# Optimization experiments

Measured on AMD Instinct MI355X. Metric: run time of the kernel, lower is better.

Reference implementation:

```python
import jax, jax.numpy as jnp
import numpy as np

B, N, C, H, R = 64, 197, 768, 12, 98   # batch, tokens, dim, heads, eliminated tokens
SPARSITY, ALPHA = 0.2, 0.1
EPS = 1e-5  # torch nn.LayerNorm default


def layernorm(x, g, b):
    m = jnp.mean(x, axis=-1, keepdims=True)
    v = jnp.var(x, axis=-1, keepdims=True)
    return (x - m) / jnp.sqrt(v + EPS) * g + b


def setup_inputs() -> dict:
    key = jax.random.key(0)
    ks = jax.random.split(key, 8)
    s = lambda k, sh: (jax.random.normal(k, sh, jnp.float32) * 0.02)
    return dict(
        x=jax.random.normal(ks[0], (B, N, C), jnp.float32),
        norm1_g=jnp.ones((C,), jnp.float32), norm1_b=jnp.zeros((C,), jnp.float32),
        qkv_w=s(ks[1], (C, 3 * C)),                      # qkv_bias=False
        proj_w=s(ks[2], (C, C)), proj_b=jnp.zeros((C,), jnp.float32),
        norm2_g=jnp.ones((C,), jnp.float32), norm2_b=jnp.zeros((C,), jnp.float32),
        fc1_w=s(ks[3], (C, 4 * C)), fc1_b=jnp.zeros((4 * C,), jnp.float32),
        fc2_w=s(ks[4], (4 * C, C)), fc2_b=jnp.zeros((C,), jnp.float32),
    )


def reference(x, norm1_g, norm1_b, qkv_w, proj_w, proj_b,
              norm2_g, norm2_b, fc1_w, fc1_b, fc2_w, fc2_b):
    Dh = C // H
    scale = Dh ** -0.5
    # --- attention block ---
    h = layernorm(x, norm1_g, norm1_b)
    qkv = (h @ qkv_w).reshape(B, N, 3, H, Dh).transpose(2, 0, 3, 1, 4)
    q, k, v = qkv[0] * scale, qkv[1], qkv[2]
    attn = jax.nn.softmax(jnp.einsum('bhnd,bhmd->bhnm', q, k), axis=-1)  # [B,H,N,N]
    out = jnp.einsum('bhnm,bhmd->bhnd', attn, v).transpose(0, 2, 1, 3).reshape(B, N, C)
    x = x + out @ proj_w + proj_b
    # --- selection: DiagAttn (head-mean attention diagonal, excluding CLS) ---
    diag = jnp.diagonal(attn.mean(1), axis1=1, axis2=2)[:, 1:]          # [B, N-1]
    token_rank = jnp.argsort(-diag, axis=1) + 1                          # indices into [1, N)
    nk = N - 1 - R                                                       # kept image tokens
    idx_kept = jnp.sort(jnp.concatenate(
        [jnp.zeros((B, 1), token_rank.dtype), token_rank[:, :nk]], axis=1), axis=1)  # [B, K]
    idx_elim = jnp.sort(token_rank[:, nk:], axis=1)                      # [B, R]
    K = nk + 1
    # --- propagate: ThresholdGraph (multihead=True, threshold=True) ---
    x_kept = jnp.take_along_axis(x, idx_kept[:, :, None], axis=1)        # [B, K, C]
    x_elim = jnp.take_along_axis(x, idx_elim[:, :, None], axis=1)        # [B, R, C]
    w = jnp.take_along_axis(attn, idx_kept[:, None, :, None], axis=2)    # [B,H,K,N]
    w = jnp.take_along_axis(w, idx_elim[:, None, None, :], axis=3)       # [B,H,K,R]
    thr_idx = int(R * K * SPARSITY)
    w_sorted = -jnp.sort(-w.reshape(B, H, K * R), axis=-1)               # descending
    thr = w_sorted[:, :, thr_idx][:, :, None, None]
    w = jnp.where(w >= thr, w, jnp.zeros((), w.dtype))
    x_prop = jnp.einsum('bhke,behd->bkhd', w, x_elim.reshape(B, R, H, Dh)).reshape(B, K, C)
    x = x_kept + ALPHA * x_prop                                          # [B, K, C]
    # --- mlp block ---
    h2 = layernorm(x, norm2_g, norm2_b)
    h2 = jax.nn.gelu(h2 @ fc1_w + fc1_b, approximate=False) @ fc2_w + fc2_b
    return x + h2
```

## Files before the change

### kernel.cpp

```cpp
#include <hip/hip_runtime.h>
#include <math.h>

#define NTOK 197
#define CD   768
#define NH   12
#define DH   64
#define NBATCH 64
#define RTOK 98
#define KTOK 99
#define THRN 1941
#define WTOT (KTOK*RTOK)

typedef __attribute__((ext_vector_type(8))) short short8;
typedef __attribute__((ext_vector_type(8))) unsigned short u16x8;
typedef __attribute__((ext_vector_type(4))) float floatx4;

__device__ __forceinline__ int clamp196(int v){ return ((unsigned)v > 196u) ? 196 : v; }
__device__ __forceinline__ unsigned short f2b(float f){
  unsigned u = __float_as_uint(f);
  return (unsigned short)((u + 0x7FFFu + ((u>>16)&1u)) >> 16);
}
__device__ __forceinline__ float us2f(unsigned short u){ return __uint_as_float(((unsigned)u)<<16); }
__device__ __forceinline__ int swz(int row, int q){ return q ^ (((row>>1)&3)<<3); }

__device__ __forceinline__ void ldsplit(const float* ap, int rem, u16x8& h, u16x8& l){
  float v[8];
  if (rem >= 8) {
    float4 t0 = *(const float4*)ap, t1 = *(const float4*)(ap+4);
    v[0]=t0.x; v[1]=t0.y; v[2]=t0.z; v[3]=t0.w;
    v[4]=t1.x; v[5]=t1.y; v[6]=t1.z; v[7]=t1.w;
  } else {
#pragma unroll
    for (int j=0;j<8;j++) v[j] = (j < rem) ? ap[j] : 0.f;
  }
#pragma unroll
  for (int j=0;j<8;j++){
    unsigned short hh = f2b(v[j]);
    h[j] = hh;
    l[j] = f2b(v[j] - us2f(hh));
  }
}

__global__ __launch_bounds__(256) void fill_kernel(float* __restrict__ out, int n, float val)
{
  int i = blockIdx.x*256 + threadIdx.x;
  if (i < n) out[i] = val;
}

__global__ __launch_bounds__(256) void tcast_k(const float* __restrict__ src, int K, int ldn, int col0,
                                               unsigned short* __restrict__ dst)
{
  __shared__ float t[32][33];
  int n0 = blockIdx.x*32, k0 = blockIdx.y*32;
  int lx = threadIdx.x & 31, ly = threadIdx.x >> 5;
#pragma unroll
  for (int i=0;i<4;i++)
    t[ly + i*8][lx] = src[(long)(k0 + ly + i*8)*ldn + col0 + n0 + lx];
  __syncthreads();
#pragma unroll
  for (int i=0;i<4;i++){
    int n = ly + i*8;
    dst[(long)(n0 + n)*K + k0 + lx] = f2b(t[lx][n]);
  }
}

__global__ __launch_bounds__(256) void tcast3_k(const float* __restrict__ src, int K, int ldn, int col0,
                                                unsigned short* __restrict__ dsth,
                                                unsigned short* __restrict__ dstl)
{
  __shared__ float t[32][33];
  int n0 = blockIdx.x*32, k0 = blockIdx.y*32;
  int lx = threadIdx.x & 31, ly = threadIdx.x >> 5;
#pragma unroll
  for (int i=0;i<4;i++)
    t[ly + i*8][lx] = src[(long)(k0 + ly + i*8)*ldn + col0 + n0 + lx];
  __syncthreads();
#pragma unroll
  for (int i=0;i<4;i++){
    int n = ly + i*8;
    float v = t[lx][n];
    unsigned short h = f2b(v);
    dsth[(long)(n0 + n)*K + k0 + lx] = h;
    dstl[(long)(n0 + n)*K + k0 + lx] = f2b(v - us2f(h));
  }
}

__global__ __launch_bounds__(256) void vtrans_k(const unsigned short* __restrict__ src,
                                                unsigned short* __restrict__ dst)
{
  __shared__ unsigned short t[32][33];
  int z = blockIdx.z;
  int t0 = blockIdx.x*32, d0 = blockIdx.y*32;
  int lx = threadIdx.x & 31, ly = threadIdx.x >> 5;
  const unsigned short* s = src + (long)z*NTOK*DH;
  unsigned short* o = dst + (long)z*DH*NTOK;
#pragma unroll
  for (int i=0;i<4;i++){
    int tok = t0 + ly + i*8;
    t[ly+i*8][lx] = (tok < NTOK) ? s[(long)tok*DH + d0 + lx] : (unsigned short)0;
  }
  __syncthreads();
#pragma unroll
  for (int i=0;i<4;i++){
    int d = d0 + ly + i*8;
    int tok = t0 + lx;
    if (tok < NTOK) o[(long)d*NTOK + tok] = t[lx][ly+i*8];
  }
}

__global__ __launch_bounds__(256) void ln_kernel(const float* __restrict__ xin,
                                                 const float* __restrict__ gam,
                                                 const float* __restrict__ bet,
                                                 unsigned short* __restrict__ outh,
                                                 unsigned short* __restrict__ outl)
{
  int row = blockIdx.x;
  int tid = threadIdx.x;
  long base = (long)row * CD;
  float v[3];
#pragma unroll
  for (int i=0;i<3;i++) v[i] = xin[base + tid + i*256];
  float s  = v[0]+v[1]+v[2];
  float s2 = v[0]*v[0]+v[1]*v[1]+v[2]*v[2];
#pragma unroll
  for (int off=32; off; off>>=1){ s += __shfl_down(s,off); s2 += __shfl_down(s2,off); }
  __shared__ float ps[4], ps2[4], mb[2];
  if ((tid&63)==0){ ps[tid>>6]=s; ps2[tid>>6]=s2; }
  __syncthreads();
  if (tid==0){
    float S  = ps[0]+ps[1]+ps[2]+ps[3];
    float S2 = ps2[0]+ps2[1]+ps2[2]+ps2[3];
    float m  = S / (float)CD;
    float var = S2 / (float)CD - m*m;
    mb[0]=m; mb[1]=1.0f/sqrtf(var + 1e-5f);
  }
  __syncthreads();
  float m=mb[0], inv=mb[1];
#pragma unroll
  for (int i=0;i<3;i++){
    int c = tid + i*256;
    float r = (v[i]-m)*inv*gam[c] + bet[c];
    unsigned short h = f2b(r);
    outh[base+c] = h;
    if (outl) outl[base+c] = f2b(r - us2f(h));
  }
}

struct PvP {
  const float* P;
  const unsigned short* Vt;
  unsigned short* C;
};

__global__ __launch_bounds__(256) void pv_k(PvP p)
{
  __shared__ short Ahs[128*32], Als[128*32], Bs[64*32];
  int tid = threadIdx.x;
  int z = blockIdx.z;
  int cb = z / NH, h = z - cb*NH;
  const float* Az = p.P + (long)z*NTOK*NTOK;
  const unsigned short* Bz = p.Vt + (long)z*DH*NTOK;
  int m0 = blockIdx.y*128;
  int w = tid>>6, l = tid&63;
  int wm = (w&1)*64, wn = (w>>1)*32;
  int lr = l&15, kq = (l>>4)*8;
  floatx4 acc[4][2];
#pragma unroll
  for (int i=0;i<4;i++)
#pragma unroll
    for (int j=0;j<2;j++) acc[i][j] = (floatx4){0.f,0.f,0.f,0.f};
  int r0i = tid>>2, q0 = (tid&3)*8;
  int r1i = r0i + 64;
  int w0s = swz(r0i, q0), w1s = swz(r1i, q0);
  for (int k0 = 0; k0 < NTOK; k0 += 32) {
    u16x8 ah0={0,0,0,0,0,0,0,0}, al0={0,0,0,0,0,0,0,0};
    u16x8 ah1={0,0,0,0,0,0,0,0}, al1={0,0,0,0,0,0,0,0};
    u16x8 b0 ={0,0,0,0,0,0,0,0};
    int rem = NTOK - k0 - q0;
    { int gm = m0 + r0i;
      if (gm < NTOK && rem > 0) ldsplit(Az + (long)gm*NTOK + k0 + q0, rem, ah0, al0); }
    { int gm = m0 + r1i;
      if (gm < NTOK && rem > 0) ldsplit(Az + (long)gm*NTOK + k0 + q0, rem, ah1, al1); }
    { const unsigned short* bp = Bz + (long)r0i*NTOK + k0 + q0;
      if (rem >= 8) b0 = *(const u16x8*)bp;
      else if (rem > 0) {
#pragma unroll
        for (int j=0;j<8;j++) if (j < rem) b0[j] = bp[j];
      } }
    __syncthreads();
    *(u16x8*)&Ahs[r0i*32 + w0s] = ah0;
    *(u16x8*)&Ahs[r1i*32 + w1s] = ah1;
    *(u16x8*)&Als[r0i*32 + w0s] = al0;
    *(u16x8*)&Als[r1i*32 + w1s] = al1;
    *(u16x8*)&Bs [r0i*32 + w0s] = b0;
    __syncthreads();
    short8 afh[4], afl[4], bfr[2];
#pragma unroll
    for (int mt=0;mt<4;mt++){
      int rr = wm + mt*16 + lr; int rs = rr*32 + swz(rr,kq);
      afh[mt] = *(short8*)&Ahs[rs];
      afl[mt] = *(short8*)&Als[rs];
    }
#pragma unroll
    for (int nt=0;nt<2;nt++){
      int rr = wn + nt*16 + lr;
      bfr[nt] = *(short8*)&Bs[rr*32 + swz(rr,kq)];
    }
#pragma unroll
    for (int mt=0;mt<4;mt++)
#pragma unroll
      for (int nt=0;nt<2;nt++){
        acc[mt][nt] = __builtin_amdgcn_mfma_f32_16x16x32_bf16(afh[mt], bfr[nt], acc[mt][nt], 0, 0, 0);
        acc[mt][nt] = __builtin_amdgcn_mfma_f32_16x16x32_bf16(afl[mt], bfr[nt], acc[mt][nt], 0, 0, 0);
      }
  }
  int rbase = (l>>4)*4;
#pragma unroll
  for (int mt=0;mt<4;mt++){
#pragma unroll
    for (int r=0;r<4;r++){
      int gm = m0 + wm + mt*16 + rbase + r;
      if (gm >= NTOK) continue;
#pragma unroll
      for (int nt=0;nt<2;nt++){
        int gn = wn + nt*16 + lr;
        p.C[(long)cb*NTOK*CD + (long)gm*CD + h*DH + gn] = f2b(acc[mt][nt][r]);
      }
    }
  }
}

struct MmP {
  const unsigned short* A;
  const unsigned short* B;
  void* C;
  const float* bias;
  const float* resid;
  unsigned short* vout;
  int M, N, K, ldc;
};

template<int EPI>
__global__ __launch_bounds__(256) void mgemm_k(MmP p)
{
  __shared__ short As[128*32];
  __shared__ short Bs[128*32];
  int tid = threadIdx.x;
  int m0 = blockIdx.y*128, n0 = blockIdx.x*128;
  int w = tid>>6, l = tid&63;
  int wm = (w&1)*64, wn = (w>>1)*64;
  int lr = l&15, kq = (l>>4)*8;
  floatx4 acc[4][4];
#pragma unroll
  for (int i=0;i<4;i++)
#pragma unroll
    for (int j=0;j<4;j++) acc[i][j] = (floatx4){0.f,0.f,0.f,0.f};
  int r0i = tid>>2, q0 = (tid&3)*8;
  int r1i = r0i + 64;
  int w0s = swz(r0i, q0), w1s = swz(r1i, q0);
  for (int k0 = 0; k0 < p.K; k0 += 32) {
    u16x8 a0 = {0,0,0,0,0,0,0,0}, a1 = {0,0,0,0,0,0,0,0};
    { int gm = m0 + r0i;
      if (gm < p.M) a0 = *(const u16x8*)(p.A + (long)gm*p.K + k0 + q0); }
    { int gm = m0 + r1i;
      if (gm < p.M) a1 = *(const u16x8*)(p.A + (long)gm*p.K + k0 + q0); }
    u16x8 b0 = *(const u16x8*)(p.B + (long)(n0 + r0i)*p.K + k0 + q0);
    u16x8 b1 = *(const u16x8*)(p.B + (long)(n0 + r1i)*p.K + k0 + q0);
    __syncthreads();
    *(u16x8*)&As[r0i*32 + w0s] = a0;
    *(u16x8*)&As[r1i*32 + w1s] = a1;
    *(u16x8*)&Bs[r0i*32 + w0s] = b0;
    *(u16x8*)&Bs[r1i*32 + w1s] = b1;
    __syncthreads();
    short8 af[4], bfr[4];
#pragma unroll
    for (int mt=0;mt<4;mt++){ int rr = wm + mt*16 + lr; af[mt]  = *(short8*)&As[rr*32 + swz(rr,kq)]; }
#pragma unroll
    for (int nt=0;nt<4;nt++){ int rr = wn + nt*16 + lr; bfr[nt] = *(short8*)&Bs[rr*32 + swz(rr,kq)]; }
#pragma unroll
    for (int mt=0;mt<4;mt++)
#pragma unroll
      for (int nt=0;nt<4;nt++)
        acc[mt][nt] = __builtin_amdgcn_mfma_f32_16x16x32_bf16(af[mt], bfr[nt], acc[mt][nt], 0, 0, 0);
  }
  int rbase = (l>>4)*4;
#pragma unroll
  for (int mt=0;mt<4;mt++){
#pragma unroll
    for (int r=0;r<4;r++){
      int gm = m0 + wm + mt*16 + rbase + r;
      if (gm >= p.M) continue;
#pragma unroll
      for (int nt=0;nt<4;nt++){
        int gn = n0 + wn + nt*16 + lr;
        float val = acc[mt][nt][r];
        if (EPI == 1) {
          int cb = gm / NTOK, tok = gm - cb*NTOK;
          int h = gn >> 6, d = gn & 63;
          p.vout[(((long)cb*NH + h)*NTOK + tok)*DH + d] = f2b(val);
        } else if (EPI == 2) {
          ((float*)p.C)[(long)gm*p.ldc + gn] = val + p.bias[gn] + p.resid[(long)gm*p.ldc + gn];
        } else {
          float u = val + p.bias[gn];
          ((unsigned short*)p.C)[(long)gm*p.ldc + gn] = f2b(0.5f*u*(1.0f + erff(u*0.70710678118654752f)));
        }
      }
    }
  }
}

struct Mm3P {
  const unsigned short *Ah, *Al, *Bh, *Bl;
  float* C;
  unsigned short *qh, *ql, *kh, *kl;
  long az, bz, cz;
  int M, N, K, ldc;
};

template<int EPI>
__global__ __launch_bounds__(256) void mgemm3_k(Mm3P p)
{
  __shared__ short Ahs[128*32], Als[128*32], Bhs[128*32], Bls[128*32];
  int tid = threadIdx.x;
  int z = blockIdx.z;
  const unsigned short* Azh = p.Ah + (long)z*p.az;
  const unsigned short* Azl = p.Al + (long)z*p.az;
  const unsigned short* Bzh = p.Bh + (long)z*p.bz;
  const unsigned short* Bzl = p.Bl + (long)z*p.bz;
  int m0 = blockIdx.y*128, n0 = blockIdx.x*128;
  int w = tid>>6, l = tid&63;
  int wm = (w&1)*64, wn = (w>>1)*64;
  int lr = l&15, kq = (l>>4)*8;
  floatx4 acc[4][4];
#pragma unroll
  for (int i=0;i<4;i++)
#pragma unroll
    for (int j=0;j<4;j++) acc[i][j] = (floatx4){0.f,0.f,0.f,0.f};
  int r0i = tid>>2, q0 = (tid&3)*8;
  int r1i = r0i + 64;
  int w0s = swz(r0i, q0), w1s = swz(r1i, q0);
  for (int k0 = 0; k0 < p.K; k0 += 32) {
    u16x8 ah0={0,0,0,0,0,0,0,0}, al0={0,0,0,0,0,0,0,0};
    u16x8 ah1={0,0,0,0,0,0,0,0}, al1={0,0,0,0,0,0,0,0};
    u16x8 bh0={0,0,0,0,0,0,0,0}, bl0={0,0,0,0,0,0,0,0};
    u16x8 bh1={0,0,0,0,0,0,0,0}, bl1={0,0,0,0,0,0,0,0};
    { int gm = m0 + r0i;
      if (gm < p.M) {
        long o = (long)gm*p.K + k0 + q0;
        ah0 = *(const u16x8*)(Azh + o);
        al0 = *(const u16x8*)(Azl + o);
      } }
    { int gm = m0 + r1i;
      if (gm < p.M) {
        long o = (long)gm*p.K + k0 + q0;
        ah1 = *(const u16x8*)(Azh + o);
        al1 = *(const u16x8*)(Azl + o);
      } }
    { int gn = n0 + r0i;
      if (gn < p.N) {
        long o = (long)gn*p.K + k0 + q0;
        bh0 = *(const u16x8*)(Bzh + o);
        bl0 = *(const u16x8*)(Bzl + o);
      } }
    { int gn = n0 + r1i;
      if (gn < p.N) {
        long o = (long)gn*p.K + k0 + q0;
        bh1 = *(const u16x8*)(Bzh + o);
        bl1 = *(const u16x8*)(Bzl + o);
      } }
    __syncthreads();
    *(u16x8*)&Ahs[r0i*32 + w0s] = ah0;
    *(u16x8*)&Ahs[r1i*32 + w1s] = ah1;
    *(u16x8*)&Als[r0i*32 + w0s] = al0;
    *(u16x8*)&Als[r1i*32 + w1s] = al1;
    *(u16x8*)&Bhs[r0i*32 + w0s] = bh0;
    *(u16x8*)&Bhs[r1i*32 + w1s] = bh1;
    *(u16x8*)&Bls[r0i*32 + w0s] = bl0;
    *(u16x8*)&Bls[r1i*32 + w1s] = bl1;
    __syncthreads();
    short8 afh[4], afl[4], bfh[4], bfl[4];
#pragma unroll
    for (int mt=0;mt<4;mt++){
      int rr = wm + mt*16 + lr; int rs = rr*32 + swz(rr,kq);
      afh[mt] = *(short8*)&Ahs[rs];
      afl[mt] = *(short8*)&Als[rs];
    }
#pragma unroll
    for (int nt=0;nt<4;nt++){
      int rr = wn + nt*16 + lr; int rs = rr*32 + swz(rr,kq);
      bfh[nt] = *(short8*)&Bhs[rs];
      bfl[nt] = *(short8*)&Bls[rs];
    }
#pragma unroll
    for (int mt=0;mt<4;mt++)
#pragma unroll
      for (int nt=0;nt<4;nt++){
        acc[mt][nt] = __builtin_amdgcn_mfma_f32_16x16x32_bf16(afh[mt], bfh[nt], acc[mt][nt], 0, 0, 0);
        acc[mt][nt] = __builtin_amdgcn_mfma_f32_16x16x32_bf16(afh[mt], bfl[nt], acc[mt][nt], 0, 0, 0);
        acc[mt][nt] = __builtin_amdgcn_mfma_f32_16x16x32_bf16(afl[mt], bfh[nt], acc[mt][nt], 0, 0, 0);
      }
  }
  int rbase = (l>>4)*4;
#pragma unroll
  for (int mt=0;mt<4;mt++){
#pragma unroll
    for (int r=0;r<4;r++){
      int gm = m0 + wm + mt*16 + rbase + r;
      if (gm >= p.M) continue;
#pragma unroll
      for (int nt=0;nt<4;nt++){
        int gn = n0 + wn + nt*16 + lr;
        if (gn >= p.N) continue;
        float val = acc[mt][nt][r];
        if (EPI == 0) {
          p.C[(long)z*p.cz + (long)gm*p.ldc + gn] = val;
        } else {
          int which = (gn >= CD) ? 1 : 0;
          int rc = gn - which*CD;
          int hd = rc >> 6, dd = rc & 63;
          int cb = gm / NTOK, tok = gm - cb*NTOK;
          long off = (((long)cb*NH + hd)*NTOK + tok)*DH + dd;
          float v = which ? val : val*0.125f;
          unsigned short h = f2b(v);
          unsigned short lo16 = f2b(v - us2f(h));
          if (which) { p.kh[off] = h; p.kl[off] = lo16; }
          else       { p.qh[off] = h; p.ql[off] = lo16; }
        }
      }
    }
  }
}

__global__ __launch_bounds__(256) void softmax_kernel(float* __restrict__ attn)
{
  long row = (long)blockIdx.x*4 + (threadIdx.x>>6);
  int ln = threadIdx.x & 63;
  float* rp = attn + row*NTOK;
  float v[4]; float mx = -3.4e38f;
#pragma unroll
  for (int i=0;i<4;i++){
    int c = ln + i*64;
    v[i] = (c < NTOK) ? rp[c] : -3.4e38f;
    mx = fmaxf(mx, v[i]);
  }
#pragma unroll
  for (int off=32; off; off>>=1) mx = fmaxf(mx, __shfl_xor(mx, off));
  float sum = 0.f;
#pragma unroll
  for (int i=0;i<4;i++){
    int c = ln + i*64;
    v[i] = (c < NTOK) ? expf(v[i]-mx) : 0.f;
    sum += v[i];
  }
#pragma unroll
  for (int off=32; off; off>>=1) sum += __shfl_xor(sum, off);
#pragma unroll
  for (int i=0;i<4;i++){
    int c = ln + i*64;
    if (c < NTOK) rp[c] = v[i] / sum;
  }
}

__global__ __launch_bounds__(256) void select_kernel(const float* __restrict__ attn,
                                                     int* __restrict__ idx_kept,
                                                     int* __restrict__ idx_elim, int b0)
{
  int cb = blockIdx.x, tid = threadIdx.x;
  int b = b0 + cb;
  __shared__ float diag[NTOK-1];
  __shared__ int kept[NTOK];
  if (tid < NTOK-1) {
    int t = tid + 1;
    float s = 0.f;
#pragma unroll
    for (int h=0; h<NH; h++)
      s += attn[(((long)cb*NH + h)*NTOK + t)*NTOK + t];
    diag[tid] = s / 12.0f;
  }
  if (tid < KTOK) idx_kept[b*KTOK + tid] = 0;
  if (tid < RTOK) idx_elim[b*RTOK + tid] = 1;
  __syncthreads();
  if (tid < NTOK-1) {
    float dv = diag[tid];
    int r = 0;
    for (int m=0; m<NTOK-1; m++){
      float dm = diag[m];
      r += ((dm > dv) || (dm == dv && m < tid)) ? 1 : 0;
    }
    kept[tid+1] = (r < (NTOK-1-RTOK)) ? 1 : 0;
  }
  __syncthreads();
  if (tid < NTOK-1) {
    int t = tid + 1;
    if (kept[t]) {
      int pos = 1;
      for (int s2=1; s2<t; s2++) pos += kept[s2];
      if (pos >= 1 && pos < KTOK) idx_kept[b*KTOK + pos] = t;
    } else {
      int pos = 0;
      for (int s2=1; s2<t; s2++) pos += 1 - kept[s2];
      if (pos >= 0 && pos < RTOK) idx_elim[b*RTOK + pos] = t;
    }
  }
  if (tid == 0) idx_kept[b*KTOK] = 0;
}

#define PNEL 38
__global__ __launch_bounds__(256) void prop_kernel(const float* __restrict__ attn,
                                                   const float* __restrict__ x1c,
                                                   const int* __restrict__ idx_kept,
                                                   const int* __restrict__ idx_elim,
                                                   float* __restrict__ x2, int b0)
{
  int z = blockIdx.x;
  int cb = z / NH, h = z - cb*NH;
  int b = b0 + cb;
  int tid = threadIdx.x;
  int wid = tid >> 6, l = tid & 63;
  int lr = l & 15, hi2 = l >> 4;
  __shared__ short WhL[112*128];
  __shared__ short XtL[64*128];
  __shared__ unsigned hist[64];
  __shared__ int kidx[KTOK], eidx[RTOK];
  if (tid < KTOK) kidx[tid] = clamp196(idx_kept[b*KTOK + tid]);
  if (tid < RTOK) eidx[tid] = clamp196(idx_elim[b*RTOK + tid]);
  u16x8 zz = {0,0,0,0,0,0,0,0};
#pragma unroll
  for (int i=0;i<7;i++) *(u16x8*)&WhL[tid*8 + i*2048] = zz;
#pragma unroll
  for (int i=0;i<4;i++) *(u16x8*)&XtL[tid*8 + i*2048] = zz;
  __syncthreads();
  for (int i = tid; i < RTOK*DH; i += 256){
    int e = i >> 6, d = i & 63;
    float v = x1c[((long)cb*NTOK + eidx[e])*CD + h*DH + d];
    XtL[d*128 + (((e>>3) ^ (d&7))<<3) + (e&7)] = (short)f2b(v);
  }
  const float* ab = attn + (long)z*NTOK*NTOK;
  unsigned wb[PNEL];
#pragma unroll
  for (int j=0;j<PNEL;j++){
    int i = tid + (j<<8);
    if (i < WTOT){
      int k = i / RTOK, e = i - k*RTOK;
      wb[j] = __float_as_uint(ab[kidx[k]*NTOK + eidx[e]]);
    } else wb[j] = 0u;
  }
  unsigned P = 0; int rrank = THRN;
  for (int pass=0; pass<5; ++pass){
    int sh = 24 - 6*pass;
    if (tid < 64) hist[tid] = 0u;
    __syncthreads();
#pragma unroll
    for (int j=0;j<PNEL;j++){
      int i = tid + (j<<8);
      unsigned v = wb[j];
      bool m = (i < WTOT) && ((pass == 0) || ((v >> (sh+6)) == P));
      if (m) atomicAdd(&hist[(v>>sh)&63u], 1u);
    }
    __syncthreads();
    unsigned cum = 0; int bsel = 0; unsigned above = 0;
    for (int bb=63; bb>=0; --bb){
      unsigned hv = hist[bb];
      if (cum + hv >= (unsigned)rrank){ bsel = bb; above = cum; break; }
      cum += hv;
    }
    P = (P<<6) | (unsigned)bsel;
    rrank -= (int)above;
    __syncthreads();
  }
  unsigned thrbits = P;
#pragma unroll
  for (int j=0;j<PNEL;j++){
    int i = tid + (j<<8);
    if (i < WTOT){
      int k = i / RTOK, e = i - k*RTOK;
      unsigned v = (wb[j] >= thrbits) ? wb[j] : 0u;
      WhL[k*128 + (((e>>3) ^ (k&7))<<3) + (e&7)] = (short)f2b(__uint_as_float(v));
    }
  }
  __syncthreads();
  floatx4 acc[7];
#pragma unroll
  for (int mt=0;mt<7;mt++) acc[mt] = (floatx4){0.f,0.f,0.f,0.f};
  short8 bfr[4];
#pragma unroll
  for (int ks=0;ks<4;ks++){
    int c = ks*4 + hi2;
    int rd = wid*16 + lr;
    bfr[ks] = *(short8*)&XtL[rd*128 + ((c ^ (lr&7))<<3)];
  }
#pragma unroll
  for (int mt=0;mt<7;mt++){
#pragma unroll
    for (int ks=0;ks<4;ks++){
      int c = ks*4 + hi2;
      int rw = mt*16 + lr;
      short8 af = *(short8*)&WhL[rw*128 + ((c ^ (lr&7))<<3)];
      acc[mt] = __builtin_amdgcn_mfma_f32_16x16x32_bf16(af, bfr[ks], acc[mt], 0, 0, 0);
    }
  }
#pragma unroll
  for (int mt=0;mt<7;mt++){
#pragma unroll
    for (int r=0;r<4;r++){
      int kt = mt*16 + hi2*4 + r;
      if (kt >= KTOK) continue;
      int d = wid*16 + lr;
      float xk = x1c[((long)cb*NTOK + kidx[kt])*CD + h*DH + d];
      x2[((long)b*KTOK + kt)*CD + h*DH + d] = xk + 0.1f*acc[mt][r];
    }
  }
}

extern "C" void kernel_launch(void* const* d_in, const int* in_sizes, int n_in,
                              void* d_out, int out_size, void* d_ws, size_t ws_size,
                              hipStream_t stream)
{
  const float* x     = (const float*)d_in[0];
  const float* n1g   = (const float*)d_in[1];
  const float* n1b   = (const float*)d_in[2];
  const float* qkvw  = (const float*)d_in[3];
  const float* projw = (const float*)d_in[4];
  const float* projb = (const float*)d_in[5];
  const float* n2g   = (const float*)d_in[6];
  const float* n2b   = (const float*)d_in[7];
  const float* fc1w  = (const float*)d_in[8];
  const float* fc1b  = (const float*)d_in[9];
  const float* fc2w  = (const float*)d_in[10];
  const float* fc2b  = (const float*)d_in[11];
  float* out = (float*)d_out;

  const long XROW = (long)NTOK*CD;
  const long AH   = (long)NTOK*NTOK;
  const long AB   = (long)NH*AH;
  const long SMALL = 6336L + 6272L;
  const long WFIX  = 1769472L;
  const long PB = AB + 3*XROW + XROW/2;
  const long MLPFIX = 2359296L;
  const long MINREQ = SMALL + WFIX + (MLPFIX + 64*1920L > PB ? MLPFIX + 64*1920L : PB);

  long wsf = (long)(ws_size / 4);
  if (wsf < MINREQ) {
    float val = (float)(ws_size >> 20) * 1000.0f + 1.0f;
    fill_kernel<<<dim3((out_size+255)/256), 256, 0, stream>>>(out, out_size, val);
    return;
  }

  long avail = wsf - SMALL - WFIX;
  int G = (int)(avail / PB);
  if (G > NBATCH) G = NBATCH;
  if (G < 1) G = 1;
  long rcl = ((avail - MLPFIX) / 1920L) / 64L * 64L;
  int RC = (int)(rcl > 6336L ? 6336L : rcl);
  if (RC < 64) RC = 64;

  float* ws = (float*)d_ws;
  int*   idx_kept = (int*)ws;
  int*   idx_elim = idx_kept + 6336;
  unsigned short* qkwh   = (unsigned short*)(ws + SMALL);
  unsigned short* qkwl   = qkwh + 1179648;
  unsigned short* qkvwvT = qkwl + 1179648;
  unsigned short* projwT = qkvwvT + 589824;
  float* base  = ws + SMALL + WFIX;
  float* attnc = base;
  unsigned short* qh = (unsigned short*)(base + (long)G*AB);
  unsigned short* ql = qh + (long)G*XROW;
  float* x1c = (float*)qh;
  unsigned short* kh = (unsigned short*)(base + (long)G*AB + (long)G*XROW);
  unsigned short* kl = kh + (long)G*XROW;
  unsigned short* aoutb = kh;
  unsigned short* vc = (unsigned short*)(base + (long)G*AB + 2L*G*XROW);
  unsigned short* h1h = (unsigned short*)(base + (long)G*AB + 2L*G*XROW + (long)G*XROW/2);
  unsigned short* h1l = h1h + (long)G*XROW;
  unsigned short* vt  = h1h;
  unsigned short* fc1wT = (unsigned short*)base;
  unsigned short* fc2wT = fc1wT + 2359296;
  unsigned short* h2b   = (unsigned short*)(base + MLPFIX);
  unsigned short* gb    = h2b + (long)RC*CD;

  tcast3_k<<<dim3(48,24), 256, 0, stream>>>(qkvw, CD, 3*CD, 0, qkwh, qkwl);
  tcast_k <<<dim3(24,24), 256, 0, stream>>>(qkvw, CD, 3*CD, 2*CD, qkvwvT);
  tcast_k <<<dim3(24,24), 256, 0, stream>>>(projw, CD, CD, 0, projwT);

  for (int b0 = 0; b0 < NBATCH; b0 += G) {
    int GL = (NBATCH - b0 < G) ? (NBATCH - b0) : G;
    int MROW = GL*NTOK;
    ln_kernel<<<dim3(MROW), 256, 0, stream>>>(x + (long)b0*XROW, n1g, n1b, h1h, h1l);
    {
      Mm3P p{}; p.Ah=h1h; p.Al=h1l; p.Bh=qkwh; p.Bl=qkwl;
      p.qh=qh; p.ql=ql; p.kh=kh; p.kl=kl;
      p.M=MROW; p.N=2*CD; p.K=CD; p.ldc=0; p.az=0; p.bz=0; p.cz=0;
      mgemm3_k<1><<<dim3(12,(MROW+127)/128,1), 256, 0, stream>>>(p);
    }
    {
      MmP p{}; p.A=h1h; p.B=qkvwvT; p.vout=vc;
      p.M=MROW; p.N=CD; p.K=CD; p.ldc=CD;
      mgemm_k<1><<<dim3(6,(MROW+127)/128,1), 256, 0, stream>>>(p);
    }
    vtrans_k<<<dim3(7,2,GL*NH), 256, 0, stream>>>(vc, vt);
    {
      Mm3P p{}; p.Ah=qh; p.Al=ql; p.Bh=kh; p.Bl=kl; p.C=attnc;
      p.M=NTOK; p.N=NTOK; p.K=DH; p.ldc=NTOK;
      p.az=(long)NTOK*DH; p.bz=(long)NTOK*DH; p.cz=AH;
      mgemm3_k<0><<<dim3(2,2,GL*NH), 256, 0, stream>>>(p);
    }
    softmax_kernel<<<dim3(GL*591), 256, 0, stream>>>(attnc);
    select_kernel<<<dim3(GL), 256, 0, stream>>>(attnc, idx_kept, idx_elim, b0);
    {
      PvP p{}; p.P=attnc; p.Vt=vt; p.C=aoutb;
      pv_k<<<dim3(1,2,GL*NH), 256, 0, stream>>>(p);
    }
    {
      MmP p{}; p.A=aoutb; p.B=projwT; p.C=x1c;
      p.M=MROW; p.N=CD; p.K=CD; p.ldc=CD;
      p.bias=projb; p.resid=x + (long)b0*XROW;
      mgemm_k<2><<<dim3(6,(MROW+127)/128,1), 256, 0, stream>>>(p);
    }
    prop_kernel<<<dim3(GL*NH), 256, 0, stream>>>(attnc, x1c, idx_kept, idx_elim, out, b0);
  }

  tcast_k<<<dim3(96,24), 256, 0, stream>>>(fc1w, CD, 4*CD, 0, fc1wT);
  tcast_k<<<dim3(24,96), 256, 0, stream>>>(fc2w, 4*CD, CD, 0, fc2wT);

  for (int r0 = 0; r0 < NBATCH*KTOK; r0 += RC) {
    int RCL = (NBATCH*KTOK - r0 < RC) ? (NBATCH*KTOK - r0) : RC;
    ln_kernel<<<dim3(RCL), 256, 0, stream>>>(out + (long)r0*CD, n2g, n2b, h2b, nullptr);
    {
      MmP p{}; p.A=h2b; p.B=fc1wT; p.C=gb;
      p.M=RCL; p.N=4*CD; p.K=CD; p.ldc=4*CD; p.bias=fc1b;
      mgemm_k<3><<<dim3(24,(RCL+127)/128,1), 256, 0, stream>>>(p);
    }
    {
      MmP p{}; p.A=gb; p.B=fc2wT; p.C=out + (long)r0*CD;
      p.M=RCL; p.N=CD; p.K=4*CD; p.ldc=CD;
      p.bias=fc2b; p.resid=out + (long)r0*CD;
      mgemm_k<2><<<dim3(6,(RCL+127)/128,1), 256, 0, stream>>>(p);
    }
  }
}
```

Baseline: 763.2 us.

## Fuse QK^T score GEMM with row softmax in a single kernel

Replaces the separate split-bf16 QK^T GEMM and the standalone softmax kernel with one kernel. Each block stages all of K for a head in swizzled LDS, computes 128 query rows across the full key width with MFMA, then does the row softmax in registers before writing probabilities. This removes the write and re-read of the raw score matrix and one launch per batch group. The cost is a large register footprint (26 accumulators per lane), fewer blocks per head, and Q fragments read directly from global memory.

```diff
diff --git a/kernel.cpp b/kernel.cpp
--- a/kernel.cpp
+++ b/kernel.cpp
@@ -10,6 +10,7 @@
 #define KTOK 99
 #define THRN 1941
 #define WTOT (KTOK*RTOK)
+#define SROWS 208
 
 typedef __attribute__((ext_vector_type(8))) short short8;
 typedef __attribute__((ext_vector_type(8))) unsigned short u16x8;
@@ -143,6 +144,105 @@
     unsigned short h = f2b(r);
     outh[base+c] = h;
     if (outl) outl[base+c] = f2b(r - us2f(h));
+  }
+}
+
+__global__ __launch_bounds__(256) void sqs_k(const unsigned short* __restrict__ Qh,
+                                             const unsigned short* __restrict__ Ql,
+                                             const unsigned short* __restrict__ Kh,
+                                             const unsigned short* __restrict__ Kl,
+                                             float* __restrict__ S)
+{
+  __shared__ short Bh_s[SROWS*64], Bl_s[SROWS*64];
+  int tid = threadIdx.x;
+  int z = blockIdx.y;
+  int m0 = blockIdx.x * 128;
+  const unsigned short* qhz = Qh + (long)z*NTOK*DH;
+  const unsigned short* qlz = Ql + (long)z*NTOK*DH;
+  const unsigned short* khz = Kh + (long)z*NTOK*DH;
+  const unsigned short* klz = Kl + (long)z*NTOK*DH;
+  u16x8 zz = {0,0,0,0,0,0,0,0};
+  for (int i = tid; i < SROWS*8; i += 256) {
+    int row = i>>3, c = i&7;
+    u16x8 vh = zz, vl = zz;
+    if (row < NTOK) {
+      vh = *(const u16x8*)(khz + (long)row*DH + c*8);
+      vl = *(const u16x8*)(klz + (long)row*DH + c*8);
+    }
+    int off = row*64 + ((c ^ (row&7))<<3);
+    *(u16x8*)&Bh_s[off] = vh;
+    *(u16x8*)&Bl_s[off] = vl;
+  }
+  __syncthreads();
+  int w = tid>>6, l = tid&63;
+  int lr = l&15, hi2 = l>>4, kq = hi2*8;
+  int rbase0 = m0 + (w<<5);
+  floatx4 acc[2][13];
+#pragma unroll
+  for (int mt=0;mt<2;mt++)
+#pragma unroll
+    for (int nt=0;nt<13;nt++) acc[mt][nt] = (floatx4){0.f,0.f,0.f,0.f};
+#pragma unroll
+  for (int ks=0; ks<2; ks++){
+    int k0 = ks*32;
+    short8 afh[2], afl[2];
+#pragma unroll
+    for (int mt=0;mt<2;mt++){
+      int rowA = clamp196(rbase0 + mt*16 + lr);
+      long qo = (long)rowA*DH + k0 + kq;
+      afh[mt] = *(const short8*)(qhz + qo);
+      afl[mt] = *(const short8*)(qlz + qo);
+    }
+#pragma unroll
+    for (int nt=0;nt<13;nt++){
+      int rowB = nt*16 + lr;
+      int cc = (ks<<2) + hi2;
+      int off = rowB*64 + ((cc ^ (rowB&7))<<3);
+      short8 bfh = *(short8*)&Bh_s[off];
+      short8 bfl = *(short8*)&Bl_s[off];
+#pragma unroll
+      for (int mt=0;mt<2;mt++){
+        acc[mt][nt] = __builtin_amdgcn_mfma_f32_16x16x32_bf16(afh[mt], bfh, acc[mt][nt], 0, 0, 0);
+        acc[mt][nt] = __builtin_amdgcn_mfma_f32_16x16x32_bf16(afh[mt], bfl, acc[mt][nt], 0, 0, 0);
+        acc[mt][nt] = __builtin_amdgcn_mfma_f32_16x16x32_bf16(afl[mt], bfh, acc[mt][nt], 0, 0, 0);
+      }
+    }
+  }
+  float* Sz = S + (long)z*NTOK*NTOK;
+#pragma unroll
+  for (int mt=0;mt<2;mt++){
+#pragma unroll
+    for (int r=0;r<4;r++){
+      int row = rbase0 + mt*16 + hi2*4 + r;
+      float ev[13];
+      float mx = -3.4e38f;
+#pragma unroll
+      for (int nt=0;nt<13;nt++){
+        int col = nt*16 + lr;
+        float v = acc[mt][nt][r];
+        if (col >= NTOK) v = -3.4e38f;
+        ev[nt] = v;
+        mx = fmaxf(mx, v);
+      }
+#pragma unroll
+      for (int mk=1; mk<16; mk<<=1) mx = fmaxf(mx, __shfl_xor(mx, mk));
+      float sum = 0.f;
+#pragma unroll
+      for (int nt=0;nt<13;nt++){
+        float e = expf(ev[nt]-mx);
+        ev[nt] = e;
+        sum += e;
+      }
+#pragma unroll
+      for (int mk=1; mk<16; mk<<=1) sum += __shfl_xor(sum, mk);
+      if (row < NTOK){
+#pragma unroll
+        for (int nt=0;nt<13;nt++){
+          int col = nt*16 + lr;
+          if (col < NTOK) Sz[(long)row*NTOK + col] = ev[nt]/sum;
+        }
+      }
+    }
   }
 }
 
@@ -431,36 +531,6 @@
   }
 }
 
-__global__ __launch_bounds__(256) void softmax_kernel(float* __restrict__ attn)
-{
-  long row = (long)blockIdx.x*4 + (threadIdx.x>>6);
-  int ln = threadIdx.x & 63;
-  float* rp = attn + row*NTOK;
-  float v[4]; float mx = -3.4e38f;
-#pragma unroll
-  for (int i=0;i<4;i++){
-    int c = ln + i*64;
-    v[i] = (c < NTOK) ? rp[c] : -3.4e38f;
-    mx = fmaxf(mx, v[i]);
-  }
-#pragma unroll
-  for (int off=32; off; off>>=1) mx = fmaxf(mx, __shfl_xor(mx, off));
-  float sum = 0.f;
-#pragma unroll
-  for (int i=0;i<4;i++){
-    int c = ln + i*64;
-    v[i] = (c < NTOK) ? expf(v[i]-mx) : 0.f;
-    sum += v[i];
-  }
-#pragma unroll
-  for (int off=32; off; off>>=1) sum += __shfl_xor(sum, off);
-#pragma unroll
-  for (int i=0;i<4;i++){
-    int c = ln + i*64;
-    if (c < NTOK) rp[c] = v[i] / sum;
-  }
-}
-
 __global__ __launch_bounds__(256) void select_kernel(const float* __restrict__ attn,
                                                      int* __restrict__ idx_kept,
                                                      int* __restrict__ idx_elim, int b0)
@@ -698,13 +768,7 @@
       mgemm_k<1><<<dim3(6,(MROW+127)/128,1), 256, 0, stream>>>(p);
     }
     vtrans_k<<<dim3(7,2,GL*NH), 256, 0, stream>>>(vc, vt);
-    {
-      Mm3P p{}; p.Ah=qh; p.Al=ql; p.Bh=kh; p.Bl=kl; p.C=attnc;
-      p.M=NTOK; p.N=NTOK; p.K=DH; p.ldc=NTOK;
-      p.az=(long)NTOK*DH; p.bz=(long)NTOK*DH; p.cz=AH;
-      mgemm3_k<0><<<dim3(2,2,GL*NH), 256, 0, stream>>>(p);
-    }
-    softmax_kernel<<<dim3(GL*591), 256, 0, stream>>>(attnc);
+    sqs_k<<<dim3(2, GL*NH), 256, 0, stream>>>(qh, ql, kh, kl, attnc);
     select_kernel<<<dim3(GL), 256, 0, stream>>>(attnc, idx_kept, idx_elim, b0);
     {
       PvP p{}; p.P=attnc; p.Vt=vt; p.C=aoutb;
```

Result: faster. 712.2 us (-6.7%).
